# Kernel optimization log

Hardware: AMD Instinct MI355X
Metric: run time of the kernel (lower is better)

The kernel has to match this reference:

```python
import jax, jax.numpy as jnp
import numpy as np

N_NODES = 100000
N_EDGES = 3200000
F_IN = 512
HIDDEN = 16
N_CLASSES = 16


def setup_inputs() -> dict:
    key = jax.random.key(0)
    k1, k2, k3, k4 = jax.random.split(key, 4)
    x = jax.random.normal(k1, (N_NODES, F_IN), dtype=jnp.float32)
    edge_index = jax.random.randint(k2, (2, N_EDGES), 0, N_NODES, dtype=jnp.int32)
    # Glorot-style init for GCN weights
    W1 = jax.random.normal(k3, (F_IN, HIDDEN), dtype=jnp.float32) * np.float32(np.sqrt(2.0 / (F_IN + HIDDEN)))
    b1 = jnp.zeros((HIDDEN,), dtype=jnp.float32)
    W2 = jax.random.normal(k4, (HIDDEN, N_CLASSES), dtype=jnp.float32) * np.float32(np.sqrt(2.0 / (HIDDEN + N_CLASSES)))
    b2 = jnp.zeros((N_CLASSES,), dtype=jnp.float32)
    return {"x": x, "W1": W1, "b1": b1, "W2": W2, "b2": b2, "edge_index": edge_index}


def _gcn_conv(x, src, dst, W, b, n_nodes):
    """PyG GCNConv: h = x @ W, then symmetric-normalized aggregation with self-loops, + bias."""
    h = x @ W  # [N, out]
    # degrees include self-loops (edge weight 1.0 everywhere)
    ones = jnp.ones(src.shape[0], dtype=h.dtype)
    deg = jax.ops.segment_sum(ones, dst, num_segments=n_nodes) + 1.0  # +1 for self-loop
    dinv = jax.lax.rsqrt(deg)  # deg >= 1, no zero guard needed
    norm = dinv[src] * dinv[dst]  # [E]
    agg = jax.ops.segment_sum(h[src] * norm[:, None], dst, num_segments=n_nodes)
    # self-loop contribution: norm_ii = 1/deg_i
    agg = agg + h * (dinv * dinv)[:, None]
    return agg + b


def reference(x, W1, b1, W2, b2, edge_index):
    src, dst = edge_index[0], edge_index[1]
    n = x.shape[0]
    h = jax.nn.relu(_gcn_conv(x, src, dst, W1, b1, n))
    # dropout is identity in eval mode
    out = _gcn_conv(h, src, dst, W2, b2, n)
    return jax.nn.log_softmax(out, axis=1)
```

## Files before the change

kernel.cpp:

```cpp
#include <hip/hip_runtime.h>
#include <hip/hip_bf16.h>
#include <math.h>

constexpr int N_NODES = 100000;
constexpr int N_EDGES = 3200000;
constexpr int F_IN    = 512;
constexpr int HID     = 16;

constexpr int NPAD = 100352;

constexpr int B_BITS = 8;
constexpr int NPB    = 1 << B_BITS;
constexpr int NBKT   = (N_NODES + NPB - 1) / NPB;
constexpr int SBLK   = 400;
constexpr int CHUNK  = N_EDGES / SBLK;
constexpr int MAX_BKT_E = 12288;

typedef float f32x4 __attribute__((ext_vector_type(4)));
typedef short bfrag8 __attribute__((ext_vector_type(8)));

__device__ __forceinline__ unsigned short f2bf_rne(float f) {
    unsigned int u = __float_as_uint(f);
    u += 0x7FFFu + ((u >> 16) & 1u);
    return (unsigned short)(u >> 16);
}
__device__ __forceinline__ float bf2f(unsigned short u) {
    return __uint_as_float((unsigned int)u << 16);
}

__global__ __launch_bounds__(1024) void bin_count_kernel(const int* __restrict__ dst,
                                                         int* __restrict__ gcnt) {
    __shared__ int cnt[NBKT];
    const int tid = threadIdx.x;
    for (int t = tid; t < NBKT; t += 1024) cnt[t] = 0;
    __syncthreads();
    const int base = blockIdx.x * CHUNK;
    for (int i = tid; i < CHUNK; i += 1024)
        atomicAdd(&cnt[dst[base + i] >> B_BITS], 1);
    __syncthreads();
    for (int t = tid; t < NBKT; t += 1024)
        if (cnt[t]) atomicAdd(&gcnt[t], cnt[t]);
}

__global__ __launch_bounds__(512) void bucket_scan_kernel(const int* __restrict__ gcnt,
                                                          int* __restrict__ bbase,
                                                          int* __restrict__ gcur) {
    __shared__ int s[512];
    const int tid = threadIdx.x;
    s[tid] = (tid < NBKT) ? gcnt[tid] : 0;
    __syncthreads();
    for (int off = 1; off < 512; off <<= 1) {
        int v = (tid >= off) ? s[tid - off] : 0;
        __syncthreads();
        s[tid] += v;
        __syncthreads();
    }
    int excl = (tid == 0) ? 0 : s[tid - 1];
    if (tid <= NBKT) bbase[tid] = excl;
    if (tid <  NBKT) gcur[tid]  = excl;
}

__global__ __launch_bounds__(1024) void bin_scatter_kernel(const int* __restrict__ src,
                                                           const int* __restrict__ dst,
                                                           int* __restrict__ gcur,
                                                           unsigned int* __restrict__ binned) {
    __shared__ int cnt[NBKT];
    __shared__ int cur[NBKT];
    const int tid = threadIdx.x;
    for (int t = tid; t < NBKT; t += 1024) cnt[t] = 0;
    __syncthreads();
    const int base = blockIdx.x * CHUNK;
    for (int i = tid; i < CHUNK; i += 1024)
        atomicAdd(&cnt[dst[base + i] >> B_BITS], 1);
    __syncthreads();
    for (int t = tid; t < NBKT; t += 1024)
        cur[t] = cnt[t] ? atomicAdd(&gcur[t], cnt[t]) : 0;
    __syncthreads();
    for (int i = tid; i < CHUNK; i += 1024) {
        int d = dst[base + i];
        int b = d >> B_BITS;
        int pos = atomicAdd(&cur[b], 1);
        binned[pos] = ((unsigned)(d & (NPB - 1)) << 24) | (unsigned)src[base + i];
    }
}

__global__ __launch_bounds__(1024) void csr_bucket_kernel(const unsigned int* __restrict__ binned,
                                                          const int* __restrict__ bbase,
                                                          int* __restrict__ row,
                                                          int* __restrict__ csr,
                                                          float* __restrict__ dinv) {
    __shared__ unsigned int eb[MAX_BKT_E];
    __shared__ int deg[NPB];
    __shared__ int pre[NPB];
    __shared__ int cur[NPB];
    const int tid = threadIdx.x;
    const int b = blockIdx.x;
    const int e0 = bbase[b];
    int ne = bbase[b + 1] - e0;
    if (ne > MAX_BKT_E) ne = MAX_BKT_E;

    if (tid < NPB) deg[tid] = 0;
    for (int i = tid; i < ne; i += 1024) eb[i] = binned[e0 + i];
    __syncthreads();
    for (int i = tid; i < ne; i += 1024)
        atomicAdd(&deg[eb[i] >> 24], 1);
    __syncthreads();
    if (tid < NPB) pre[tid] = deg[tid];
    __syncthreads();
    for (int off = 1; off < NPB; off <<= 1) {
        int v = 0;
        if (tid < NPB && tid >= off) v = pre[tid - off];
        __syncthreads();
        if (tid < NPB) pre[tid] += v;
        __syncthreads();
    }
    if (tid < NPB) {
        int excl = (tid == 0) ? 0 : pre[tid - 1];
        int g = e0 + excl;
        cur[tid] = g;
        int node = b * NPB + tid;
        if (node < N_NODES) {
            row[node] = g;
            dinv[node] = rsqrtf((float)deg[tid] + 1.0f);
        }
    }
    if (b == 0 && tid == 0) row[N_NODES] = N_EDGES;
    __syncthreads();
    for (int i = tid; i < ne; i += 1024) {
        unsigned int v = eb[i];
        int pos = atomicAdd(&cur[v >> 24], 1);
        csr[pos] = (int)(v & 0xFFFFFFu);
    }
}

__global__ __launch_bounds__(256) void w1prep_kernel(const float* __restrict__ W1,
                                                     unsigned short* __restrict__ w1t) {
    int i = blockIdx.x * 256 + threadIdx.x;
    if (i < F_IN * HID) {
        int k = i >> 4, n = i & 15;
        w1t[n * F_IN + k] = f2bf_rne(W1[i]);
    }
}

__global__ __launch_bounds__(256) void gemm1_kernel(const float* __restrict__ x,
                                                    const unsigned short* __restrict__ w1t,
                                                    const float* __restrict__ b1,
                                                    const float* __restrict__ dinv,
                                                    unsigned short* __restrict__ hh_bf,
                                                    float* __restrict__ aggs1) {
    const int tid  = threadIdx.x;
    const int lane = tid & 63;
    const int wv   = tid >> 6;
    const int m    = lane & 15;
    const int quad = lane >> 4;
    const int node0 = blockIdx.x * 64 + wv * 16;

    int gm = node0 + m; if (gm >= N_NODES) gm = N_NODES - 1;
    const float* arow = x + (size_t)gm * F_IN + quad * 8;

    bfrag8 bfr[16];
    const unsigned short* wbase = w1t + m * F_IN + quad * 8;
    #pragma unroll
    for (int t = 0; t < 16; ++t)
        bfr[t] = *(const bfrag8*)(wbase + t * 32);

    f32x4 acc = {0.f, 0.f, 0.f, 0.f};
    #pragma unroll 4
    for (int t = 0; t < 16; ++t) {
        float4 lo = *(const float4*)(arow + t * 32);
        float4 hi = *(const float4*)(arow + t * 32 + 4);
        bfrag8 afr;
        afr[0] = (short)f2bf_rne(lo.x); afr[1] = (short)f2bf_rne(lo.y);
        afr[2] = (short)f2bf_rne(lo.z); afr[3] = (short)f2bf_rne(lo.w);
        afr[4] = (short)f2bf_rne(hi.x); afr[5] = (short)f2bf_rne(hi.y);
        afr[6] = (short)f2bf_rne(hi.z); afr[7] = (short)f2bf_rne(hi.w);
        acc = __builtin_amdgcn_mfma_f32_16x16x32_bf16(afr, bfr[t], acc, 0, 0, 0);
    }

    const float b1j = b1[m];
    #pragma unroll
    for (int r = 0; r < 4; ++r) {
        int gn = node0 + quad * 4 + r;
        if (gn < N_NODES) {
            float dv = dinv[gn];
            float hv = acc[r] * dv;
            size_t o = (size_t)gn * 16 + m;
            hh_bf[o] = f2bf_rne(hv);
            aggs1[o] = hv * dv + b1j;
        }
    }
}

__global__ __launch_bounds__(256) void pull1_kernel(const unsigned short* __restrict__ hh_bf,
                                                    const float* __restrict__ aggs1,
                                                    const float* __restrict__ dinv,
                                                    const int* __restrict__ row,
                                                    const int* __restrict__ csr,
                                                    const float* __restrict__ W2,
                                                    const float* __restrict__ b2,
                                                    unsigned short* __restrict__ hh2_bf,
                                                    float* __restrict__ aggs2) {
    __shared__ float w2s[256];
    __shared__ float b2s[16];
    const int tid = threadIdx.x;
    w2s[tid] = W2[tid];
    if (tid < 16) b2s[tid] = b2[tid];
    __syncthreads();

    int t = blockIdx.x * 256 + tid;
    int node = t >> 4;
    int j = t & 15;
    int p = row[node], end = row[node + 1];
    float a0 = 0.f, a1 = 0.f, a2 = 0.f, a3 = 0.f;
    for (; p + 4 <= end; p += 4) {
        int s0 = csr[p], s1 = csr[p + 1], s2 = csr[p + 2], s3 = csr[p + 3];
        a0 += bf2f(hh_bf[(s0 << 4) + j]);
        a1 += bf2f(hh_bf[(s1 << 4) + j]);
        a2 += bf2f(hh_bf[(s2 << 4) + j]);
        a3 += bf2f(hh_bf[(s3 << 4) + j]);
    }
    for (; p < end; ++p) a0 += bf2f(hh_bf[(csr[p] << 4) + j]);
    float dv = dinv[node];
    float aj = aggs1[(node << 4) + j] + dv * ((a0 + a1) + (a2 + a3));
    float vj = fmaxf(aj, 0.f);

    float h2 = 0.f;
    #pragma unroll
    for (int k = 0; k < 16; ++k) {
        float vk = __shfl(vj, k, 16);
        h2 += vk * w2s[k * 16 + j];
    }
    size_t o = (size_t)node * 16 + j;
    float hv = h2 * dv;
    hh2_bf[o] = f2bf_rne(hv);
    aggs2[o] = hv * dv + b2s[j];
}

__global__ __launch_bounds__(256) void pull2_kernel(const unsigned short* __restrict__ hh2_bf,
                                                    const float* __restrict__ aggs2,
                                                    const float* __restrict__ dinv,
                                                    const int* __restrict__ row,
                                                    const int* __restrict__ csr,
                                                    float* __restrict__ out) {
    int t = blockIdx.x * 256 + threadIdx.x;
    int node = t >> 4;
    int j = t & 15;
    int p = row[node], end = row[node + 1];
    float a0 = 0.f, a1 = 0.f, a2 = 0.f, a3 = 0.f;
    for (; p + 4 <= end; p += 4) {
        int s0 = csr[p], s1 = csr[p + 1], s2 = csr[p + 2], s3 = csr[p + 3];
        a0 += bf2f(hh2_bf[(s0 << 4) + j]);
        a1 += bf2f(hh2_bf[(s1 << 4) + j]);
        a2 += bf2f(hh2_bf[(s2 << 4) + j]);
        a3 += bf2f(hh2_bf[(s3 << 4) + j]);
    }
    for (; p < end; ++p) a0 += bf2f(hh2_bf[(csr[p] << 4) + j]);
    float oj = aggs2[(node << 4) + j] + dinv[node] * ((a0 + a1) + (a2 + a3));

    float mx = oj;
    mx = fmaxf(mx, __shfl_xor(mx, 1));
    mx = fmaxf(mx, __shfl_xor(mx, 2));
    mx = fmaxf(mx, __shfl_xor(mx, 4));
    mx = fmaxf(mx, __shfl_xor(mx, 8));
    float e = expf(oj - mx);
    float s = e;
    s += __shfl_xor(s, 1);
    s += __shfl_xor(s, 2);
    s += __shfl_xor(s, 4);
    s += __shfl_xor(s, 8);
    out[(size_t)node * 16 + j] = oj - mx - logf(s);
}

extern "C" void kernel_launch(void* const* d_in, const int* in_sizes, int n_in,
                              void* d_out, int out_size, void* d_ws, size_t ws_size,
                              hipStream_t stream) {
    const float* x    = (const float*)d_in[0];
    const float* W1   = (const float*)d_in[1];
    const float* b1   = (const float*)d_in[2];
    const float* W2   = (const float*)d_in[3];
    const float* b2   = (const float*)d_in[4];
    const int*   ei   = (const int*)d_in[5];
    const int*   src  = ei;
    const int*   dst  = ei + N_EDGES;
    float* out = (float*)d_out;

    int*   wsi  = (int*)d_ws;
    float* wsf  = (float*)d_ws;
    int*   gcnt  = wsi;
    int*   bbase = wsi + 512;
    int*   gcur  = wsi + 1024;
    float* dinv  = wsf + 2048;
    int*   row   = wsi + 2048 + NPAD;
    int*   csr   = wsi + 2048 + 2 * NPAD;
    unsigned int* binned = (unsigned int*)csr;
    const size_t off0 = 2048 + 2 * (size_t)NPAD + N_EDGES;
    unsigned short* hh_bf  = (unsigned short*)(wsi + off0);
    float*          aggs1  = wsf + off0 + 800000;
    unsigned short* hh2_bf = (unsigned short*)(wsi + off0 + 2400000);
    float*          aggs2  = wsf + off0 + 3200000;
    unsigned short* w1t    = (unsigned short*)(wsi + off0 + 4800000);

    const int GB = N_NODES / 16;
    const int MB = (N_NODES + 63) / 64;

    hipMemsetAsync(gcnt, 0, NBKT * sizeof(int), stream);
    bin_count_kernel <<<SBLK, 1024, 0, stream>>>(dst, gcnt);
    bucket_scan_kernel<<<1, 512, 0, stream>>>(gcnt, bbase, gcur);
    bin_scatter_kernel<<<SBLK, 1024, 0, stream>>>(src, dst, gcur, binned);
    csr_bucket_kernel<<<NBKT, 1024, 0, stream>>>(binned, bbase, row, csr, dinv);
    w1prep_kernel<<<32, 256, 0, stream>>>(W1, w1t);
    gemm1_kernel<<<MB, 256, 0, stream>>>(x, w1t, b1, dinv, hh_bf, aggs1);
    pull1_kernel<<<GB, 256, 0, stream>>>(hh_bf, aggs1, dinv, row, csr, W2, b2, hh2_bf, aggs2);
    pull2_kernel<<<GB, 256, 0, stream>>>(hh2_bf, aggs2, dinv, row, csr, out);
}
```

Baseline: 483.7 us.

## Use fixed-capacity buckets, padded CSR rows, and vectorized 4-lane-per-node gathers

Replaces the count/scan binning passes with fixed-capacity per-bucket slots, so edges are scattered in one pass and the separate count kernel, scan kernel and memset go away. CSR rows are padded to multiples of four using a dummy zero node, which lets both aggregation kernels use int4 index loads and ushort4 feature gathers with four lanes per node instead of sixteen. The scatter kernel also stages src/dst in LDS, and the small setup kernels are merged into one prep kernel. In exchange, correctness now depends on no bucket exceeding the fixed capacity, and the padded CSR adds some extra gather work.

Result: faster. 438.4 us (-9.4%).

```diff
diff --git a/kernel.cpp b/kernel.cpp
--- a/kernel.cpp
+++ b/kernel.cpp
@@ -1,5 +1,4 @@
 #include <hip/hip_runtime.h>
-#include <hip/hip_bf16.h>
 #include <math.h>
 
 constexpr int N_NODES = 100000;
@@ -14,7 +13,7 @@
 constexpr int NBKT   = (N_NODES + NPB - 1) / NPB;
 constexpr int SBLK   = 400;
 constexpr int CHUNK  = N_EDGES / SBLK;
-constexpr int MAX_BKT_E = 12288;
+constexpr int CAP    = 10240;
 
 typedef float f32x4 __attribute__((ext_vector_type(4)));
 typedef short bfrag8 __attribute__((ext_vector_type(8)));
@@ -28,76 +27,69 @@
     return __uint_as_float((unsigned int)u << 16);
 }
 
-__global__ __launch_bounds__(1024) void bin_count_kernel(const int* __restrict__ dst,
-                                                         int* __restrict__ gcnt) {
-    __shared__ int cnt[NBKT];
-    const int tid = threadIdx.x;
-    for (int t = tid; t < NBKT; t += 1024) cnt[t] = 0;
-    __syncthreads();
-    const int base = blockIdx.x * CHUNK;
-    for (int i = tid; i < CHUNK; i += 1024)
-        atomicAdd(&cnt[dst[base + i] >> B_BITS], 1);
-    __syncthreads();
-    for (int t = tid; t < NBKT; t += 1024)
-        if (cnt[t]) atomicAdd(&gcnt[t], cnt[t]);
-}
-
-__global__ __launch_bounds__(512) void bucket_scan_kernel(const int* __restrict__ gcnt,
-                                                          int* __restrict__ bbase,
-                                                          int* __restrict__ gcur) {
-    __shared__ int s[512];
-    const int tid = threadIdx.x;
-    s[tid] = (tid < NBKT) ? gcnt[tid] : 0;
-    __syncthreads();
-    for (int off = 1; off < 512; off <<= 1) {
-        int v = (tid >= off) ? s[tid - off] : 0;
-        __syncthreads();
-        s[tid] += v;
-        __syncthreads();
-    }
-    int excl = (tid == 0) ? 0 : s[tid - 1];
-    if (tid <= NBKT) bbase[tid] = excl;
-    if (tid <  NBKT) gcur[tid]  = excl;
+__global__ __launch_bounds__(256) void prep_kernel(const float* __restrict__ W1,
+                                                   unsigned short* __restrict__ w1t,
+                                                   int* __restrict__ gcur,
+                                                   unsigned short* __restrict__ hh_bf,
+                                                   unsigned short* __restrict__ hh2_bf) {
+    int i = blockIdx.x * 256 + threadIdx.x;
+    if (i < F_IN * HID) {
+        int k = i >> 4, n = i & 15;
+        w1t[n * F_IN + k] = f2bf_rne(W1[i]);
+    }
+    if (i < NBKT) gcur[i] = i * CAP;
+    if (i < 16) {
+        hh_bf [N_NODES * 16 + i] = 0;
+        hh2_bf[N_NODES * 16 + i] = 0;
+    }
 }
 
 __global__ __launch_bounds__(1024) void bin_scatter_kernel(const int* __restrict__ src,
                                                            const int* __restrict__ dst,
                                                            int* __restrict__ gcur,
                                                            unsigned int* __restrict__ binned) {
+    __shared__ int sdst[CHUNK];
+    __shared__ int ssrc[CHUNK];
     __shared__ int cnt[NBKT];
     __shared__ int cur[NBKT];
     const int tid = threadIdx.x;
     for (int t = tid; t < NBKT; t += 1024) cnt[t] = 0;
-    __syncthreads();
     const int base = blockIdx.x * CHUNK;
+    for (int i = tid; i < CHUNK; i += 1024) {
+        sdst[i] = dst[base + i];
+        ssrc[i] = src[base + i];
+    }
+    __syncthreads();
     for (int i = tid; i < CHUNK; i += 1024)
-        atomicAdd(&cnt[dst[base + i] >> B_BITS], 1);
+        atomicAdd(&cnt[sdst[i] >> B_BITS], 1);
     __syncthreads();
     for (int t = tid; t < NBKT; t += 1024)
         cur[t] = cnt[t] ? atomicAdd(&gcur[t], cnt[t]) : 0;
     __syncthreads();
     for (int i = tid; i < CHUNK; i += 1024) {
-        int d = dst[base + i];
+        int d = sdst[i];
         int b = d >> B_BITS;
         int pos = atomicAdd(&cur[b], 1);
-        binned[pos] = ((unsigned)(d & (NPB - 1)) << 24) | (unsigned)src[base + i];
+        binned[pos] = ((unsigned)(d & (NPB - 1)) << 24) | (unsigned)ssrc[i];
     }
 }
 
 __global__ __launch_bounds__(1024) void csr_bucket_kernel(const unsigned int* __restrict__ binned,
-                                                          const int* __restrict__ bbase,
+                                                          const int* __restrict__ gcur,
                                                           int* __restrict__ row,
+                                                          int* __restrict__ rowe,
                                                           int* __restrict__ csr,
                                                           float* __restrict__ dinv) {
-    __shared__ unsigned int eb[MAX_BKT_E];
+    __shared__ unsigned int eb[CAP];
     __shared__ int deg[NPB];
     __shared__ int pre[NPB];
     __shared__ int cur[NPB];
     const int tid = threadIdx.x;
     const int b = blockIdx.x;
-    const int e0 = bbase[b];
-    int ne = bbase[b + 1] - e0;
-    if (ne > MAX_BKT_E) ne = MAX_BKT_E;
+    const int e0 = b * CAP;
+    int ne = gcur[b] - e0;
+    if (ne > CAP) ne = CAP;
+    if (ne < 0) ne = 0;
 
     if (tid < NPB) deg[tid] = 0;
     for (int i = tid; i < ne; i += 1024) eb[i] = binned[e0 + i];
@@ -105,7 +97,7 @@
     for (int i = tid; i < ne; i += 1024)
         atomicAdd(&deg[eb[i] >> 24], 1);
     __syncthreads();
-    if (tid < NPB) pre[tid] = deg[tid];
+    if (tid < NPB) pre[tid] = (deg[tid] + 3) & ~3;
     __syncthreads();
     for (int off = 1; off < NPB; off <<= 1) {
         int v = 0;
@@ -116,29 +108,30 @@
     }
     if (tid < NPB) {
         int excl = (tid == 0) ? 0 : pre[tid - 1];
-        int g = e0 + excl;
-        cur[tid] = g;
+        int start = e0 + excl;
+        cur[tid] = start;
         int node = b * NPB + tid;
         if (node < N_NODES) {
-            row[node] = g;
+            int pd = (deg[tid] + 3) & ~3;
+            row[node]  = start;
+            rowe[node] = start + pd;
             dinv[node] = rsqrtf((float)deg[tid] + 1.0f);
         }
     }
-    if (b == 0 && tid == 0) row[N_NODES] = N_EDGES;
     __syncthreads();
     for (int i = tid; i < ne; i += 1024) {
         unsigned int v = eb[i];
         int pos = atomicAdd(&cur[v >> 24], 1);
         csr[pos] = (int)(v & 0xFFFFFFu);
     }
-}
-
-__global__ __launch_bounds__(256) void w1prep_kernel(const float* __restrict__ W1,
-                                                     unsigned short* __restrict__ w1t) {
-    int i = blockIdx.x * 256 + threadIdx.x;
-    if (i < F_IN * HID) {
-        int k = i >> 4, n = i & 15;
-        w1t[n * F_IN + k] = f2bf_rne(W1[i]);
+    if (tid < NPB) {
+        int node = b * NPB + tid;
+        if (node < N_NODES) {
+            int d = deg[tid];
+            int pd = (d + 3) & ~3;
+            int s = e0 + ((tid == 0) ? 0 : pre[tid - 1]) + d;
+            for (int q = d; q < pd; ++q) csr[s++] = N_NODES;
+        }
     }
 }
 
@@ -195,80 +188,107 @@
                                                     const float* __restrict__ aggs1,
                                                     const float* __restrict__ dinv,
                                                     const int* __restrict__ row,
+                                                    const int* __restrict__ rowe,
                                                     const int* __restrict__ csr,
                                                     const float* __restrict__ W2,
                                                     const float* __restrict__ b2,
                                                     unsigned short* __restrict__ hh2_bf,
                                                     float* __restrict__ aggs2) {
-    __shared__ float w2s[256];
-    __shared__ float b2s[16];
+    __shared__ f32x4 w2s[64];
+    __shared__ f32x4 b2s[4];
     const int tid = threadIdx.x;
-    w2s[tid] = W2[tid];
-    if (tid < 16) b2s[tid] = b2[tid];
+    if (tid < 64) w2s[tid] = ((const f32x4*)W2)[tid];
+    if (tid < 4)  b2s[tid] = ((const f32x4*)b2)[tid];
     __syncthreads();
 
     int t = blockIdx.x * 256 + tid;
-    int node = t >> 4;
-    int j = t & 15;
-    int p = row[node], end = row[node + 1];
-    float a0 = 0.f, a1 = 0.f, a2 = 0.f, a3 = 0.f;
-    for (; p + 4 <= end; p += 4) {
-        int s0 = csr[p], s1 = csr[p + 1], s2 = csr[p + 2], s3 = csr[p + 3];
-        a0 += bf2f(hh_bf[(s0 << 4) + j]);
-        a1 += bf2f(hh_bf[(s1 << 4) + j]);
-        a2 += bf2f(hh_bf[(s2 << 4) + j]);
-        a3 += bf2f(hh_bf[(s3 << 4) + j]);
-    }
-    for (; p < end; ++p) a0 += bf2f(hh_bf[(csr[p] << 4) + j]);
+    int node = t >> 2;
+    int l = t & 3;
+    if (node >= N_NODES) return;
+
+    int p = row[node], e = rowe[node];
+    const unsigned short* hb = hh_bf + (l << 2);
+    f32x4 a0 = {0,0,0,0}, a1 = {0,0,0,0}, a2 = {0,0,0,0}, a3 = {0,0,0,0};
+    for (; p < e; p += 4) {
+        int4 s = *(const int4*)(csr + p);
+        ushort4 g0 = *(const ushort4*)(hb + (s.x << 4));
+        ushort4 g1 = *(const ushort4*)(hb + (s.y << 4));
+        ushort4 g2 = *(const ushort4*)(hb + (s.z << 4));
+        ushort4 g3 = *(const ushort4*)(hb + (s.w << 4));
+        a0.x += bf2f(g0.x); a0.y += bf2f(g0.y); a0.z += bf2f(g0.z); a0.w += bf2f(g0.w);
+        a1.x += bf2f(g1.x); a1.y += bf2f(g1.y); a1.z += bf2f(g1.z); a1.w += bf2f(g1.w);
+        a2.x += bf2f(g2.x); a2.y += bf2f(g2.y); a2.z += bf2f(g2.z); a2.w += bf2f(g2.w);
+        a3.x += bf2f(g3.x); a3.y += bf2f(g3.y); a3.z += bf2f(g3.z); a3.w += bf2f(g3.w);
+    }
+    f32x4 a = (a0 + a1) + (a2 + a3);
     float dv = dinv[node];
-    float aj = aggs1[(node << 4) + j] + dv * ((a0 + a1) + (a2 + a3));
-    float vj = fmaxf(aj, 0.f);
-
-    float h2 = 0.f;
+    f32x4 base = *(const f32x4*)(aggs1 + ((size_t)node << 4) + (l << 2));
+    float v[4];
+    #pragma unroll
+    for (int c = 0; c < 4; ++c) v[c] = fmaxf(base[c] + dv * a[c], 0.f);
+
+    f32x4 h2 = {0.f, 0.f, 0.f, 0.f};
     #pragma unroll
     for (int k = 0; k < 16; ++k) {
-        float vk = __shfl(vj, k, 16);
-        h2 += vk * w2s[k * 16 + j];
-    }
-    size_t o = (size_t)node * 16 + j;
-    float hv = h2 * dv;
-    hh2_bf[o] = f2bf_rne(hv);
-    aggs2[o] = hv * dv + b2s[j];
+        float vk = __shfl(v[k & 3], k >> 2, 4);
+        f32x4 w = w2s[k * 4 + l];
+        h2.x += vk * w.x; h2.y += vk * w.y; h2.z += vk * w.z; h2.w += vk * w.w;
+    }
+    f32x4 bb = b2s[l];
+    ushort4 hs;
+    f32x4 ag;
+    float hv0 = h2.x * dv; hs.x = f2bf_rne(hv0); ag.x = hv0 * dv + bb.x;
+    float hv1 = h2.y * dv; hs.y = f2bf_rne(hv1); ag.y = hv1 * dv + bb.y;
+    float hv2 = h2.z * dv; hs.z = f2bf_rne(hv2); ag.z = hv2 * dv + bb.z;
+    float hv3 = h2.w * dv; hs.w = f2bf_rne(hv3); ag.w = hv3 * dv + bb.w;
+    size_t o = ((size_t)node << 4) + (l << 2);
+    *(ushort4*)(hh2_bf + o) = hs;
+    *(f32x4*)(aggs2 + o) = ag;
 }
 
 __global__ __launch_bounds__(256) void pull2_kernel(const unsigned short* __restrict__ hh2_bf,
                                                     const float* __restrict__ aggs2,
                                                     const float* __restrict__ dinv,
                                                     const int* __restrict__ row,
+                                                    const int* __restrict__ rowe,
                                                     const int* __restrict__ csr,
                                                     float* __restrict__ out) {
     int t = blockIdx.x * 256 + threadIdx.x;
-    int node = t >> 4;
-    int j = t & 15;
-    int p = row[node], end = row[node + 1];
-    float a0 = 0.f, a1 = 0.f, a2 = 0.f, a3 = 0.f;
-    for (; p + 4 <= end; p += 4) {
-        int s0 = csr[p], s1 = csr[p + 1], s2 = csr[p + 2], s3 = csr[p + 3];
-        a0 += bf2f(hh2_bf[(s0 << 4) + j]);
-        a1 += bf2f(hh2_bf[(s1 << 4) + j]);
-        a2 += bf2f(hh2_bf[(s2 << 4) + j]);
-        a3 += bf2f(hh2_bf[(s3 << 4) + j]);
-    }
-    for (; p < end; ++p) a0 += bf2f(hh2_bf[(csr[p] << 4) + j]);
-    float oj = aggs2[(node << 4) + j] + dinv[node] * ((a0 + a1) + (a2 + a3));
-
-    float mx = oj;
-    mx = fmaxf(mx, __shfl_xor(mx, 1));
-    mx = fmaxf(mx, __shfl_xor(mx, 2));
-    mx = fmaxf(mx, __shfl_xor(mx, 4));
-    mx = fmaxf(mx, __shfl_xor(mx, 8));
-    float e = expf(oj - mx);
-    float s = e;
+    int node = t >> 2;
+    int l = t & 3;
+    if (node >= N_NODES) return;
+
+    int p = row[node], e = rowe[node];
+    const unsigned short* hb = hh2_bf + (l << 2);
+    f32x4 a0 = {0,0,0,0}, a1 = {0,0,0,0}, a2 = {0,0,0,0}, a3 = {0,0,0,0};
+    for (; p < e; p += 4) {
+        int4 s = *(const int4*)(csr + p);
+        ushort4 g0 = *(const ushort4*)(hb + (s.x << 4));
+        ushort4 g1 = *(const ushort4*)(hb + (s.y << 4));
+        ushort4 g2 = *(const ushort4*)(hb + (s.z << 4));
+        ushort4 g3 = *(const ushort4*)(hb + (s.w << 4));
+        a0.x += bf2f(g0.x); a0.y += bf2f(g0.y); a0.z += bf2f(g0.z); a0.w += bf2f(g0.w);
+        a1.x += bf2f(g1.x); a1.y += bf2f(g1.y); a1.z += bf2f(g1.z); a1.w += bf2f(g1.w);
+        a2.x += bf2f(g2.x); a2.y += bf2f(g2.y); a2.z += bf2f(g2.z); a2.w += bf2f(g2.w);
+        a3.x += bf2f(g3.x); a3.y += bf2f(g3.y); a3.z += bf2f(g3.z); a3.w += bf2f(g3.w);
+    }
+    f32x4 a = (a0 + a1) + (a2 + a3);
+    float dv = dinv[node];
+    f32x4 base = *(const f32x4*)(aggs2 + ((size_t)node << 4) + (l << 2));
+    f32x4 o4;
+    o4.x = base.x + dv * a.x; o4.y = base.y + dv * a.y;
+    o4.z = base.z + dv * a.z; o4.w = base.w + dv * a.w;
+
+    float m = fmaxf(fmaxf(o4.x, o4.y), fmaxf(o4.z, o4.w));
+    m = fmaxf(m, __shfl_xor(m, 1));
+    m = fmaxf(m, __shfl_xor(m, 2));
+    float s = expf(o4.x - m) + expf(o4.y - m) + expf(o4.z - m) + expf(o4.w - m);
     s += __shfl_xor(s, 1);
     s += __shfl_xor(s, 2);
-    s += __shfl_xor(s, 4);
-    s += __shfl_xor(s, 8);
-    out[(size_t)node * 16 + j] = oj - mx - logf(s);
+    float ls = m + logf(s);
+    f32x4 r;
+    r.x = o4.x - ls; r.y = o4.y - ls; r.z = o4.z - ls; r.w = o4.w - ls;
+    *(f32x4*)(out + ((size_t)node << 4) + (l << 2)) = r;
 }
 
 extern "C" void kernel_launch(void* const* d_in, const int* in_sizes, int n_in,
@@ -284,32 +304,38 @@
     const int*   dst  = ei + N_EDGES;
     float* out = (float*)d_out;
 
+    constexpr size_t SLOTS    = (size_t)NBKT * CAP;
+    constexpr size_t OFF_DINV = 512;
+    constexpr size_t OFF_ROW  = 512 + (size_t)NPAD;
+    constexpr size_t OFF_ROWE = 512 + 2 * (size_t)NPAD;
+    constexpr size_t OFF_CSR  = 512 + 3 * (size_t)NPAD;
+    constexpr size_t OFF_HH   = OFF_CSR + SLOTS;
+    constexpr size_t OFF_AG1  = OFF_HH + 800512;
+    constexpr size_t OFF_HH2  = OFF_AG1 + 1600000;
+    constexpr size_t OFF_AG2  = OFF_HH2 + 800512;
+    constexpr size_t OFF_W1T  = OFF_AG2 + 1600000;
+
     int*   wsi  = (int*)d_ws;
     float* wsf  = (float*)d_ws;
-    int*   gcnt  = wsi;
-    int*   bbase = wsi + 512;
-    int*   gcur  = wsi + 1024;
-    float* dinv  = wsf + 2048;
-    int*   row   = wsi + 2048 + NPAD;
-    int*   csr   = wsi + 2048 + 2 * NPAD;
+    int*   gcur  = wsi;
+    float* dinv  = wsf + OFF_DINV;
+    int*   row   = wsi + OFF_ROW;
+    int*   rowe  = wsi + OFF_ROWE;
+    int*   csr   = wsi + OFF_CSR;
     unsigned int* binned = (unsigned int*)csr;
-    const size_t off0 = 2048 + 2 * (size_t)NPAD + N_EDGES;
-    unsigned short* hh_bf  = (unsigned short*)(wsi + off0);
-    float*          aggs1  = wsf + off0 + 800000;
-    unsigned short* hh2_bf = (unsigned short*)(wsi + off0 + 2400000);
-    float*          aggs2  = wsf + off0 + 3200000;
-    unsigned short* w1t    = (unsigned short*)(wsi + off0 + 4800000);
-
-    const int GB = N_NODES / 16;
-    const int MB = (N_NODES + 63) / 64;
-
-    hipMemsetAsync(gcnt, 0, NBKT * sizeof(int), stream);
-    bin_count_kernel <<<SBLK, 1024, 0, stream>>>(dst, gcnt);
-    bucket_scan_kernel<<<1, 512, 0, stream>>>(gcnt, bbase, gcur);
+    unsigned short* hh_bf  = (unsigned short*)(wsi + OFF_HH);
+    float*          aggs1  = wsf + OFF_AG1;
+    unsigned short* hh2_bf = (unsigned short*)(wsi + OFF_HH2);
+    float*          aggs2  = wsf + OFF_AG2;
+    unsigned short* w1t    = (unsigned short*)(wsi + OFF_W1T);
+
+    const int MB  = (N_NODES + 63) / 64;
+    const int GB4 = (N_NODES * 4 + 255) / 256;
+
+    prep_kernel       <<<32, 256, 0, stream>>>(W1, w1t, gcur, hh_bf, hh2_bf);
     bin_scatter_kernel<<<SBLK, 1024, 0, stream>>>(src, dst, gcur, binned);
-    csr_bucket_kernel<<<NBKT, 1024, 0, stream>>>(binned, bbase, row, csr, dinv);
-    w1prep_kernel<<<32, 256, 0, stream>>>(W1, w1t);
-    gemm1_kernel<<<MB, 256, 0, stream>>>(x, w1t, b1, dinv, hh_bf, aggs1);
-    pull1_kernel<<<GB, 256, 0, stream>>>(hh_bf, aggs1, dinv, row, csr, W2, b2, hh2_bf, aggs2);
-    pull2_kernel<<<GB, 256, 0, stream>>>(hh2_bf, aggs2, dinv, row, csr, out);
-}
+    csr_bucket_kernel <<<NBKT, 1024, 0, stream>>>(binned, gcur, row, rowe, csr, dinv);
+    gemm1_kernel      <<<MB, 256, 0, stream>>>(x, w1t, b1, dinv, hh_bf, aggs1);
+    pull1_kernel      <<<GB4, 256, 0, stream>>>(hh_bf, aggs1, dinv, row, rowe, csr, W2, b2, hh2_bf, aggs2);
+    pull2_kernel      <<<GB4, 256, 0, stream>>>(hh2_bf, aggs2, dinv, row, rowe, csr, out);
+}
```
